# Optimization experiments

Measured on AMD Instinct MI355X. Metric: run time of the kernel, lower is better.

## Reference

```python
import jax, jax.numpy as jnp
import numpy as np

IN_FEATURES = 4096
OUT_FEATURES = 4096
NUM_GROUPS = 16
GROUP_IN = IN_FEATURES // NUM_GROUPS    # 256
GROUP_OUT = OUT_FEATURES // NUM_GROUPS  # 256
BATCH = 8192


def setup_inputs() -> dict:
    key = jax.random.key(0)
    kx, kw, kb = jax.random.split(key, 3)
    x = jax.random.normal(kx, (BATCH, IN_FEATURES), dtype=jnp.float32)
    # nn.Linear weight is [out, in]; stack per-group -> [G, dout_g, din_g]
    bound = 1.0 / np.sqrt(GROUP_IN)
    W = jax.random.uniform(kw, (NUM_GROUPS, GROUP_OUT, GROUP_IN), dtype=jnp.float32,
                           minval=-bound, maxval=bound)
    b = jax.random.uniform(kb, (NUM_GROUPS, GROUP_OUT), dtype=jnp.float32,
                           minval=-bound, maxval=bound)
    return {"x": x, "W": W, "b": b}


def reference(x, W, b):
    B = x.shape[0]
    # split along features -> [B, G, din_g]; block-diagonal matmul as batched GEMM
    xg = x.reshape(B, NUM_GROUPS, GROUP_IN)
    # y[b,g,o] = sum_i xg[b,g,i] * W[g,o,i] + b[g,o]
    yg = jnp.einsum('bgi,goi->bgo', xg, W) + b
    return yg.reshape(B, OUT_FEATURES)
```

## Files before the change

### kernel.cpp

```cpp
#include <hip/hip_runtime.h>
#include <hip/hip_bf16.h>
#include <stdint.h>


#define IN_F   4096
#define OUT_F  4096
#define GIN    256
#define GOUT   256

#define BM 128
#define BN 128
#define BK 64
#define KTOT 256

using short8  = __attribute__((ext_vector_type(8))) short;
using floatx4 = __attribute__((ext_vector_type(4))) float;

__device__ __forceinline__ short f2bf_rne(float f) {
    unsigned u = __builtin_bit_cast(unsigned, f);
    unsigned r = u + 0x7FFFu + ((u >> 16) & 1u);
    return (short)(r >> 16);
}

__global__ __launch_bounds__(256, 2)
void grouped_linear_kernel(const float* __restrict__ X,
                           const float* __restrict__ W,
                           const float* __restrict__ Bias,
                           float* __restrict__ Out) {
    __shared__ __align__(16) short lsA[BM * BK];
    __shared__ __align__(16) short lsB[BN * BK];

    const int t    = threadIdx.x;
    const int lane = t & 63;
    const int wave = t >> 6;
    const int wm   = wave >> 1;
    const int wn   = wave & 1;
    const int lrow = lane & 15;
    const int quad = lane >> 4;

    const int bn   = blockIdx.x & 31;
    const int bm   = blockIdx.x >> 5;
    const int g    = bn >> 1;
    const int row0 = bm * BM;
    const int col0 = bn * BN;
    const int nlb  = (bn & 1) * BN;

    const float* Wg = W + (size_t)g * GOUT * GIN + (size_t)nlb * GIN;
    const float* Xg = X + (size_t)row0 * IN_F + g * GIN;

    floatx4 acc[4][4];
    #pragma unroll
    for (int i = 0; i < 4; ++i)
        #pragma unroll
        for (int j = 0; j < 4; ++j)
            acc[i][j] = (floatx4){0.f, 0.f, 0.f, 0.f};

    const int c8 = (t & 7) * 8;
    const int q0 = (t & 7);

    for (int kt = 0; kt < KTOT / BK; ++kt) {
        const int kbase = kt * BK;

        #pragma unroll
        for (int i = 0; i < 4; ++i) {
            int r = (t >> 3) + 32 * i;
            const float* src = Xg + (size_t)r * IN_F + kbase + c8;
            floatx4 f0 = *(const floatx4*)src;
            floatx4 f1 = *(const floatx4*)(src + 4);
            short8 p;
            p[0] = f2bf_rne(f0[0]); p[1] = f2bf_rne(f0[1]);
            p[2] = f2bf_rne(f0[2]); p[3] = f2bf_rne(f0[3]);
            p[4] = f2bf_rne(f1[0]); p[5] = f2bf_rne(f1[1]);
            p[6] = f2bf_rne(f1[2]); p[7] = f2bf_rne(f1[3]);
            int q = q0 ^ (r & 7);
            *(short8*)&lsA[r * BK + q * 8] = p;
        }
        #pragma unroll
        for (int i = 0; i < 4; ++i) {
            int n = (t >> 3) + 32 * i;
            const float* src = Wg + (size_t)n * GIN + kbase + c8;
            floatx4 f0 = *(const floatx4*)src;
            floatx4 f1 = *(const floatx4*)(src + 4);
            short8 p;
            p[0] = f2bf_rne(f0[0]); p[1] = f2bf_rne(f0[1]);
            p[2] = f2bf_rne(f0[2]); p[3] = f2bf_rne(f0[3]);
            p[4] = f2bf_rne(f1[0]); p[5] = f2bf_rne(f1[1]);
            p[6] = f2bf_rne(f1[2]); p[7] = f2bf_rne(f1[3]);
            int q = q0 ^ (n & 7);
            *(short8*)&lsB[n * BK + q * 8] = p;
        }
        __syncthreads();

        #pragma unroll
        for (int kk = 0; kk < 2; ++kk) {
            int kb = kk * 32 + quad * 8;
            int qs = kb >> 3;
            short8 a[4], b[4];
            #pragma unroll
            for (int i = 0; i < 4; ++i) {
                int r = wm * 64 + i * 16 + lrow;
                a[i] = *(const short8*)&lsA[r * BK + ((qs ^ (r & 7)) * 8)];
            }
            #pragma unroll
            for (int j = 0; j < 4; ++j) {
                int n = wn * 64 + j * 16 + lrow;
                b[j] = *(const short8*)&lsB[n * BK + ((qs ^ (n & 7)) * 8)];
            }
            #pragma unroll
            for (int i = 0; i < 4; ++i)
                #pragma unroll
                for (int j = 0; j < 4; ++j)
                    acc[i][j] = __builtin_amdgcn_mfma_f32_16x16x32_bf16(
                        a[i], b[j], acc[i][j], 0, 0, 0);
        }
        __syncthreads();
    }

    #pragma unroll
    for (int j = 0; j < 4; ++j) {
        int gc = col0 + wn * 64 + j * 16 + lrow;
        float bias = Bias[gc];
        #pragma unroll
        for (int i = 0; i < 4; ++i) {
            int gr = row0 + wm * 64 + i * 16 + quad * 4;
            floatx4 v = acc[i][j];
            #pragma unroll
            for (int rg = 0; rg < 4; ++rg)
                Out[(size_t)(gr + rg) * OUT_F + gc] = v[rg] + bias;
        }
    }
}

extern "C" void kernel_launch(void* const* d_in, const int* in_sizes, int n_in,
                              void* d_out, int out_size, void* d_ws, size_t ws_size,
                              hipStream_t stream) {
    const float* X    = (const float*)d_in[0];
    const float* W    = (const float*)d_in[1];
    const float* Bias = (const float*)d_in[2];
    float*       Out  = (float*)d_out;

    dim3 grid(64 * 32);
    dim3 block(256);
    grouped_linear_kernel<<<grid, block, 0, stream>>>(X, W, Bias, Out);
}
```

Measured before the change: 273.7 us.

## Stage X via async global-to-LDS loads with double buffering, load W directly to registers

X tiles are copied into a double-buffered fp32 LDS area with global_load_lds, so the next K-tile's load overlaps the MFMA work on the current one; bf16 conversion moves to LDS-read time. W fragments are loaded straight from global into registers per wave, skipping the LDS staging for B. The extra barrier per iteration is removed. This costs more LDS (fp32, two buffers, about 64KB per block), which may limit occupancy. W loads are now repeated across the waves that share columns. Correctness depends on the async LDS writes being complete before the barrier.

```diff
diff --git a/kernel.cpp b/kernel.cpp
--- a/kernel.cpp
+++ b/kernel.cpp
@@ -1,5 +1,4 @@
 #include <hip/hip_runtime.h>
-#include <hip/hip_bf16.h>
 #include <stdint.h>
 
 
@@ -11,10 +10,13 @@
 #define BM 128
 #define BN 128
 #define BK 64
-#define KTOT 256
+#define NK 4
 
 using short8  = __attribute__((ext_vector_type(8))) short;
 using floatx4 = __attribute__((ext_vector_type(4))) float;
+
+#define GLOBAL_AS __attribute__((address_space(1)))
+#define LDS_AS    __attribute__((address_space(3)))
 
 __device__ __forceinline__ short f2bf_rne(float f) {
     unsigned u = __builtin_bit_cast(unsigned, f);
@@ -22,13 +24,21 @@
     return (short)(r >> 16);
 }
 
+__device__ __forceinline__ short8 pack8(floatx4 f0, floatx4 f1) {
+    short8 p;
+    p[0] = f2bf_rne(f0[0]); p[1] = f2bf_rne(f0[1]);
+    p[2] = f2bf_rne(f0[2]); p[3] = f2bf_rne(f0[3]);
+    p[4] = f2bf_rne(f1[0]); p[5] = f2bf_rne(f1[1]);
+    p[6] = f2bf_rne(f1[2]); p[7] = f2bf_rne(f1[3]);
+    return p;
+}
+
 __global__ __launch_bounds__(256, 2)
 void grouped_linear_kernel(const float* __restrict__ X,
                            const float* __restrict__ W,
                            const float* __restrict__ Bias,
                            float* __restrict__ Out) {
-    __shared__ __align__(16) short lsA[BM * BK];
-    __shared__ __align__(16) short lsB[BN * BK];
+    __shared__ __align__(16) float lsA[2][BM * BK];
 
     const int t    = threadIdx.x;
     const int lane = t & 63;
@@ -55,65 +65,69 @@
         for (int j = 0; j < 4; ++j)
             acc[i][j] = (floatx4){0.f, 0.f, 0.f, 0.f};
 
-    const int c8 = (t & 7) * 8;
-    const int q0 = (t & 7);
+    auto stage = [&](int kt, int b) {
+        const int kbase = kt * BK;
+        #pragma unroll
+        for (int i = 0; i < 8; ++i) {
+            int ig   = wave * 8 + i;
+            int row  = ig * 4 + (lane >> 4);
+            int gsrc = (lane & 15) ^ (row & 15);
+            const float* src = Xg + (size_t)row * IN_F + kbase + gsrc * 4;
+            float* dst = &lsA[b][ig * 256];
+            __builtin_amdgcn_global_load_lds((const GLOBAL_AS void*)src,
+                                             (LDS_AS void*)dst, 16, 0, 0);
+        }
+    };
 
-    for (int kt = 0; kt < KTOT / BK; ++kt) {
+    stage(0, 0);
+    __syncthreads();
+
+    for (int kt = 0; kt < NK; ++kt) {
         const int kbase = kt * BK;
 
+        floatx4 braw[2][4][2];
         #pragma unroll
-        for (int i = 0; i < 4; ++i) {
-            int r = (t >> 3) + 32 * i;
-            const float* src = Xg + (size_t)r * IN_F + kbase + c8;
-            floatx4 f0 = *(const floatx4*)src;
-            floatx4 f1 = *(const floatx4*)(src + 4);
-            short8 p;
-            p[0] = f2bf_rne(f0[0]); p[1] = f2bf_rne(f0[1]);
-            p[2] = f2bf_rne(f0[2]); p[3] = f2bf_rne(f0[3]);
-            p[4] = f2bf_rne(f1[0]); p[5] = f2bf_rne(f1[1]);
-            p[6] = f2bf_rne(f1[2]); p[7] = f2bf_rne(f1[3]);
-            int q = q0 ^ (r & 7);
-            *(short8*)&lsA[r * BK + q * 8] = p;
-        }
-        #pragma unroll
-        for (int i = 0; i < 4; ++i) {
-            int n = (t >> 3) + 32 * i;
-            const float* src = Wg + (size_t)n * GIN + kbase + c8;
-            floatx4 f0 = *(const floatx4*)src;
-            floatx4 f1 = *(const floatx4*)(src + 4);
-            short8 p;
-            p[0] = f2bf_rne(f0[0]); p[1] = f2bf_rne(f0[1]);
-            p[2] = f2bf_rne(f0[2]); p[3] = f2bf_rne(f0[3]);
-            p[4] = f2bf_rne(f1[0]); p[5] = f2bf_rne(f1[1]);
-            p[6] = f2bf_rne(f1[2]); p[7] = f2bf_rne(f1[3]);
-            int q = q0 ^ (n & 7);
-            *(short8*)&lsB[n * BK + q * 8] = p;
-        }
-        __syncthreads();
-
-        #pragma unroll
-        for (int kk = 0; kk < 2; ++kk) {
-            int kb = kk * 32 + quad * 8;
-            int qs = kb >> 3;
-            short8 a[4], b[4];
-            #pragma unroll
-            for (int i = 0; i < 4; ++i) {
-                int r = wm * 64 + i * 16 + lrow;
-                a[i] = *(const short8*)&lsA[r * BK + ((qs ^ (r & 7)) * 8)];
-            }
+        for (int kk = 0; kk < 2; ++kk)
             #pragma unroll
             for (int j = 0; j < 4; ++j) {
                 int n = wn * 64 + j * 16 + lrow;
-                b[j] = *(const short8*)&lsB[n * BK + ((qs ^ (n & 7)) * 8)];
+                const float* src = Wg + (size_t)n * GIN + kbase + kk * 32 + quad * 8;
+                braw[kk][j][0] = *(const floatx4*)src;
+                braw[kk][j][1] = *(const floatx4*)(src + 4);
+            }
+
+        if (kt + 1 < NK) stage(kt + 1, (kt + 1) & 1);
+
+        short8 bfr[2][4];
+        #pragma unroll
+        for (int kk = 0; kk < 2; ++kk)
+            #pragma unroll
+            for (int j = 0; j < 4; ++j)
+                bfr[kk][j] = pack8(braw[kk][j][0], braw[kk][j][1]);
+
+        const float* buf = lsA[kt & 1];
+        #pragma unroll
+        for (int kk = 0; kk < 2; ++kk) {
+            short8 a[4];
+            #pragma unroll
+            for (int i = 0; i < 4; ++i) {
+                int row = wm * 64 + i * 16 + lrow;
+                int s0  = kk * 8 + quad * 2;
+                int g0  = s0 ^ (row & 15);
+                int g1  = (s0 + 1) ^ (row & 15);
+                floatx4 f0 = *(const floatx4*)&buf[row * 64 + g0 * 4];
+                floatx4 f1 = *(const floatx4*)&buf[row * 64 + g1 * 4];
+                a[i] = pack8(f0, f1);
             }
             #pragma unroll
             for (int i = 0; i < 4; ++i)
                 #pragma unroll
                 for (int j = 0; j < 4; ++j)
                     acc[i][j] = __builtin_amdgcn_mfma_f32_16x16x32_bf16(
-                        a[i], b[j], acc[i][j], 0, 0, 0);
+                        a[i], bfr[kk][j], acc[i][j], 0, 0, 0);
         }
-        __syncthreads();
+
+        if (kt + 1 < NK) __syncthreads();
     }
 
     #pragma unroll
```

New measurement: 276.8 us. No clear change (+1.1%).

## Keep weight slice resident in LDS and stream X directly into registers

Applied to the files above, without the earlier changes.

Each block now loads its full 128x256 weight slice once into padded LDS and loops over four 128-row M tiles. The X operand is read straight from global memory into registers in MFMA fragment layout, double-buffered one k-step ahead, so the A-side LDS staging and the per-k-step barriers go away. The grid shrinks by a factor of four so weights are converted and staged fewer times. The cost is fewer blocks, which may underfill the GPU, and uncoalesced per-lane 32-byte X reads plus higher register pressure.

```diff
diff --git a/kernel.cpp b/kernel.cpp
--- a/kernel.cpp
+++ b/kernel.cpp
@@ -1,5 +1,4 @@
 #include <hip/hip_runtime.h>
-#include <hip/hip_bf16.h>
 #include <stdint.h>
 
 
@@ -8,10 +7,10 @@
 #define GIN    256
 #define GOUT   256
 
-#define BM 128
-#define BN 128
-#define BK 64
-#define KTOT 256
+#define BN   128
+#define MT   128
+#define NMT  4
+#define LDB  264
 
 using short8  = __attribute__((ext_vector_type(8))) short;
 using floatx4 = __attribute__((ext_vector_type(4))) float;
@@ -22,13 +21,21 @@
     return (short)(r >> 16);
 }
 
+__device__ __forceinline__ short8 pack8(floatx4 f0, floatx4 f1) {
+    short8 p;
+    p[0] = f2bf_rne(f0[0]); p[1] = f2bf_rne(f0[1]);
+    p[2] = f2bf_rne(f0[2]); p[3] = f2bf_rne(f0[3]);
+    p[4] = f2bf_rne(f1[0]); p[5] = f2bf_rne(f1[1]);
+    p[6] = f2bf_rne(f1[2]); p[7] = f2bf_rne(f1[3]);
+    return p;
+}
+
 __global__ __launch_bounds__(256, 2)
 void grouped_linear_kernel(const float* __restrict__ X,
                            const float* __restrict__ W,
                            const float* __restrict__ Bias,
                            float* __restrict__ Out) {
-    __shared__ __align__(16) short lsA[BM * BK];
-    __shared__ __align__(16) short lsB[BN * BK];
+    __shared__ __align__(16) short lsB[BN * LDB];
 
     const int t    = threadIdx.x;
     const int lane = t & 63;
@@ -39,14 +46,47 @@
     const int quad = lane >> 4;
 
     const int bn   = blockIdx.x & 31;
-    const int bm   = blockIdx.x >> 5;
+    const int mb   = blockIdx.x >> 5;
     const int g    = bn >> 1;
-    const int row0 = bm * BM;
+    const int nlb  = (bn & 1) * BN;
+    const int row0 = mb * (MT * NMT);
     const int col0 = bn * BN;
-    const int nlb  = (bn & 1) * BN;
 
     const float* Wg = W + (size_t)g * GOUT * GIN + (size_t)nlb * GIN;
     const float* Xg = X + (size_t)row0 * IN_F + g * GIN;
+
+    const float* pA[4];
+    #pragma unroll
+    for (int i = 0; i < 4; ++i)
+        pA[i] = Xg + (size_t)(wm * 64 + i * 16 + lrow) * IN_F + quad * 8;
+
+    floatx4 araw[2][4][2];
+    #pragma unroll
+    for (int i = 0; i < 4; ++i) {
+        araw[0][i][0] = *(const floatx4*)(pA[i]);
+        araw[0][i][1] = *(const floatx4*)(pA[i] + 4);
+    }
+
+    #pragma unroll
+    for (int it = 0; it < 16; ++it) {
+        int G  = it * 256 + t;
+        int n  = G >> 5;
+        int gr = G & 31;
+        const float* src = Wg + (size_t)n * GIN + gr * 8;
+        floatx4 f0 = *(const floatx4*)src;
+        floatx4 f1 = *(const floatx4*)(src + 4);
+        *(short8*)&lsB[n * LDB + gr * 8] = pack8(f0, f1);
+    }
+
+    float bias[4];
+    #pragma unroll
+    for (int j = 0; j < 4; ++j)
+        bias[j] = Bias[g * GOUT + nlb + wn * 64 + j * 16 + lrow];
+
+    __syncthreads();
+
+    const int bbase = (wn * 64 + lrow) * LDB + quad * 8;
+    float* Outp = Out + (size_t)row0 * OUT_F + col0;
 
     floatx4 acc[4][4];
     #pragma unroll
@@ -55,78 +95,49 @@
         for (int j = 0; j < 4; ++j)
             acc[i][j] = (floatx4){0.f, 0.f, 0.f, 0.f};
 
-    const int c8 = (t & 7) * 8;
-    const int q0 = (t & 7);
-
-    for (int kt = 0; kt < KTOT / BK; ++kt) {
-        const int kbase = kt * BK;
-
+    for (int m = 0; m < NMT; ++m) {
         #pragma unroll
-        for (int i = 0; i < 4; ++i) {
-            int r = (t >> 3) + 32 * i;
-            const float* src = Xg + (size_t)r * IN_F + kbase + c8;
-            floatx4 f0 = *(const floatx4*)src;
-            floatx4 f1 = *(const floatx4*)(src + 4);
-            short8 p;
-            p[0] = f2bf_rne(f0[0]); p[1] = f2bf_rne(f0[1]);
-            p[2] = f2bf_rne(f0[2]); p[3] = f2bf_rne(f0[3]);
-            p[4] = f2bf_rne(f1[0]); p[5] = f2bf_rne(f1[1]);
-            p[6] = f2bf_rne(f1[2]); p[7] = f2bf_rne(f1[3]);
-            int q = q0 ^ (r & 7);
-            *(short8*)&lsA[r * BK + q * 8] = p;
-        }
-        #pragma unroll
-        for (int i = 0; i < 4; ++i) {
-            int n = (t >> 3) + 32 * i;
-            const float* src = Wg + (size_t)n * GIN + kbase + c8;
-            floatx4 f0 = *(const floatx4*)src;
-            floatx4 f1 = *(const floatx4*)(src + 4);
-            short8 p;
-            p[0] = f2bf_rne(f0[0]); p[1] = f2bf_rne(f0[1]);
-            p[2] = f2bf_rne(f0[2]); p[3] = f2bf_rne(f0[3]);
-            p[4] = f2bf_rne(f1[0]); p[5] = f2bf_rne(f1[1]);
-            p[6] = f2bf_rne(f1[2]); p[7] = f2bf_rne(f1[3]);
-            int q = q0 ^ (n & 7);
-            *(short8*)&lsB[n * BK + q * 8] = p;
-        }
-        __syncthreads();
-
-        #pragma unroll
-        for (int kk = 0; kk < 2; ++kk) {
-            int kb = kk * 32 + quad * 8;
-            int qs = kb >> 3;
-            short8 a[4], b[4];
+        for (int kk = 0; kk < 8; ++kk) {
+            if (kk == 7) {
+                #pragma unroll
+                for (int i = 0; i < 4; ++i) pA[i] += (size_t)MT * IN_F;
+            }
+            if (!(m == NMT - 1 && kk == 7)) {
+                const int nk = (kk + 1) & 7;
+                #pragma unroll
+                for (int i = 0; i < 4; ++i) {
+                    araw[(kk + 1) & 1][i][0] = *(const floatx4*)(pA[i] + nk * 32);
+                    araw[(kk + 1) & 1][i][1] = *(const floatx4*)(pA[i] + nk * 32 + 4);
+                }
+            }
+            short8 bf[4];
             #pragma unroll
-            for (int i = 0; i < 4; ++i) {
-                int r = wm * 64 + i * 16 + lrow;
-                a[i] = *(const short8*)&lsA[r * BK + ((qs ^ (r & 7)) * 8)];
-            }
+            for (int j = 0; j < 4; ++j)
+                bf[j] = *(const short8*)&lsB[bbase + j * 16 * LDB + kk * 32];
+            short8 a[4];
             #pragma unroll
-            for (int j = 0; j < 4; ++j) {
-                int n = wn * 64 + j * 16 + lrow;
-                b[j] = *(const short8*)&lsB[n * BK + ((qs ^ (n & 7)) * 8)];
-            }
+            for (int i = 0; i < 4; ++i)
+                a[i] = pack8(araw[kk & 1][i][0], araw[kk & 1][i][1]);
             #pragma unroll
             for (int i = 0; i < 4; ++i)
                 #pragma unroll
                 for (int j = 0; j < 4; ++j)
                     acc[i][j] = __builtin_amdgcn_mfma_f32_16x16x32_bf16(
-                        a[i], b[j], acc[i][j], 0, 0, 0);
+                        a[i], bf[j], acc[i][j], 0, 0, 0);
         }
-        __syncthreads();
-    }
 
-    #pragma unroll
-    for (int j = 0; j < 4; ++j) {
-        int gc = col0 + wn * 64 + j * 16 + lrow;
-        float bias = Bias[gc];
         #pragma unroll
-        for (int i = 0; i < 4; ++i) {
-            int gr = row0 + wm * 64 + i * 16 + quad * 4;
-            floatx4 v = acc[i][j];
+        for (int j = 0; j < 4; ++j) {
+            int gc = wn * 64 + j * 16 + lrow;
             #pragma unroll
-            for (int rg = 0; rg < 4; ++rg)
-                Out[(size_t)(gr + rg) * OUT_F + gc] = v[rg] + bias;
+            for (int i = 0; i < 4; ++i) {
+                int gr0 = m * MT + wm * 64 + i * 16 + quad * 4;
+                floatx4 v = acc[i][j];
+                #pragma unroll
+                for (int rg = 0; rg < 4; ++rg)
+                    Outp[(size_t)(gr0 + rg) * OUT_F + gc] = v[rg] + bias[j];
+                acc[i][j] = (floatx4){0.f, 0.f, 0.f, 0.f};
+            }
         }
     }
 }
@@ -139,7 +150,7 @@
     const float* Bias = (const float*)d_in[2];
     float*       Out  = (float*)d_out;
 
-    dim3 grid(64 * 32);
+    dim3 grid(32 * 16);
     dim3 block(256);
     grouped_linear_kernel<<<grid, block, 0, stream>>>(X, W, Bias, Out);
 }
```

Result: slower. 298.6 us (+9.1%).
